# Optimization experiments

Hardware: AMD Instinct MI355X
Metric: run time of the kernel (lower is better)

## Reference

```python
import math
import jax, jax.numpy as jnp
import numpy as np


def setup_inputs() -> dict:
    key = jax.random.key(0)
    kq, kk, kv = jax.random.split(key, 3)
    bs, n_tok, n_heads, width = 2, 2048, 8, 64
    deg = 32  # neighbors per dst token -> coo_cnt_max
    q = jax.random.normal(kq, (bs, n_tok, n_heads, width), dtype=jnp.float32)
    k = jax.random.normal(kk, (bs, n_tok, n_heads, width), dtype=jnp.float32)
    v = jax.random.normal(kv, (bs, n_tok, n_heads, width), dtype=jnp.float32)
    rng = np.random.default_rng(0)
    dst = np.repeat(np.arange(n_tok), deg)            # [cl]
    src = rng.integers(0, n_tok, size=n_tok * deg)    # [cl]
    sm = np.tile(np.arange(deg), n_tok)               # [cl], unique per dst
    coo = jnp.asarray(np.stack([dst, src, sm], axis=1), dtype=jnp.int32)  # [cl,3]
    return {"q": q, "k": k, "v": v, "coo": coo, "coo_cnt_max": deg}


def reference(q, k, v, coo, coo_cnt_max):
    bs, n_tok, n_heads, width = q.shape
    dst, src, sm = coo[:, 0], coo[:, 1], coo[:, 2]
    # [b, h, t, w] layout
    qq = q.transpose(0, 2, 1, 3)
    kk = k.transpose(0, 2, 1, 3)
    vv = v.transpose(0, 2, 1, 3)
    scale = -1.0 / math.sqrt(width)
    # per-edge negative scaled L1 distance: [b, h, cl]
    ww = jnp.sum(jnp.abs(qq[:, :, dst, :] - kk[:, :, src, :]), axis=-1) * scale
    neg_big = jnp.asarray(-1e32, dtype=q.dtype)
    # scatter edge scores into dense padded attention slots: [b, h, t, cnt+1]
    attn = jnp.full((bs, n_heads, n_tok, coo_cnt_max + 1), neg_big, dtype=q.dtype)
    attn = attn.at[:, :, dst, sm].set(ww)
    attn_sm = jax.nn.softmax(attn, axis=-1)
    # scatter values into padded neighbor-value tensor: [b, h, t, cnt+1, w]
    vw = jnp.zeros((bs, n_heads, n_tok, coo_cnt_max + 1, width), dtype=q.dtype)
    vw = vw.at[:, :, dst, sm, :].set(vv[:, :, src, :])
    vo = jnp.einsum('bhds,bhdsw->bdhw', attn_sm, vw)
    # only dst tokens appearing in coo receive output; others stay zero
    vout = jnp.zeros_like(v).at[:, dst, :, :].set(vo[:, dst, :, :])
    return vout
```

## Files before the change

kernel.cpp:

```cpp
#include <hip/hip_runtime.h>

#define BS   2
#define NT   2048
#define NH   8
#define WD   64
#define DEG  32
#define HHW  (4 * WD)
#define ROWF 260

__global__ __launch_bounds__(128) void l1attn_sparse_kernel(
    const float* __restrict__ q,
    const float* __restrict__ k,
    const float* __restrict__ v,
    const int* __restrict__ coo,
    float* __restrict__ out)
{
    const int bid   = blockIdx.x;
    const int combo = bid & 3;
    const int hh    = combo & 1;
    const int b     = combo >> 1;
    const int t     = ((bid >> 3) << 1) | ((bid >> 2) & 1);
    const int tid   = threadIdx.x;
    const int hw    = tid >> 5;
    const int l     = tid & 31;

    __shared__ int   s_src[DEG];
    __shared__ float s_q[HHW];
    __shared__ float s_k[DEG * ROWF];

    if (tid < DEG) {
        s_src[tid] = coo[(t * DEG + tid) * 3 + 1];
    }
    {
        const float2* qrow = (const float2*)
            (q + ((size_t)(b * NT + t) * NH + hh * 4) * WD);
        float2 qv = qrow[tid];
        s_q[2 * tid]     = qv.x;
        s_q[2 * tid + 1] = qv.y;
    }
    __syncthreads();

    {
        const int wv = tid >> 6;
        const int ln = tid & 63;
        #pragma unroll
        for (int r = 0; r < 16; ++r) {
            const int j = wv * 16 + r;
            const int s = s_src[j];
            const float* gaddr = k + ((size_t)(b * NT + s) * NH + hh * 4) * WD
                               + ln * 4;
            float* laddr = s_k + j * ROWF;
            __builtin_amdgcn_global_load_lds(
                (const __attribute__((address_space(1))) void*)gaddr,
                (__attribute__((address_space(3))) void*)laddr,
                16, 0, 0);
        }
    }

    const int h  = hh * 4 + hw;
    const int jg = l >> 4;
    const int wq = l & 15;
    float4 vr[16];
    #pragma unroll
    for (int i = 0; i < 16; ++i) {
        const int sv = s_src[2 * i + jg];
        vr[i] = *(const float4*)(v + ((size_t)(b * NT + sv) * NH + h) * WD + 4 * wq);
    }

    __syncthreads();

    const float* qh = s_q + hw * WD;
    float acc = 0.f;
    #pragma unroll
    for (int i = 0; i < 16; ++i) {
        float4 kv = *(const float4*)(s_k + l * ROWF + hw * WD + i * 4);
        const int wb = i * 4;
        acc += fabsf(qh[wb]     - kv.x);
        acc += fabsf(qh[wb + 1] - kv.y);
        acc += fabsf(qh[wb + 2] - kv.z);
        acc += fabsf(qh[wb + 3] - kv.w);
    }
    float logit = -0.125f * acc;

    float m = logit;
    #pragma unroll
    for (int d = 16; d >= 1; d >>= 1) m = fmaxf(m, __shfl_xor(m, d));
    float e = __expf(logit - m);
    float ssum = e;
    #pragma unroll
    for (int d = 16; d >= 1; d >>= 1) ssum += __shfl_xor(ssum, d);
    const float p = e / ssum;

    float4 o4 = make_float4(0.f, 0.f, 0.f, 0.f);
    #pragma unroll
    for (int i = 0; i < 16; ++i) {
        const float pj = __shfl(p, 2 * i + jg, 32);
        o4.x += pj * vr[i].x;
        o4.y += pj * vr[i].y;
        o4.z += pj * vr[i].z;
        o4.w += pj * vr[i].w;
    }
    o4.x += __shfl_xor(o4.x, 16);
    o4.y += __shfl_xor(o4.y, 16);
    o4.z += __shfl_xor(o4.z, 16);
    o4.w += __shfl_xor(o4.w, 16);

    if (jg == 0) {
        *(float4*)(out + ((size_t)(b * NT + t) * NH + h) * WD + 4 * wq) = o4;
    }
}

extern "C" void kernel_launch(void* const* d_in, const int* in_sizes, int n_in,
                              void* d_out, int out_size, void* d_ws, size_t ws_size,
                              hipStream_t stream) {
    const float* q   = (const float*)d_in[0];
    const float* k   = (const float*)d_in[1];
    const float* v   = (const float*)d_in[2];
    const int*   coo = (const int*)d_in[3];
    float*       o   = (float*)d_out;

    dim3 grid(BS * NT * 2);
    dim3 block(128);
    hipLaunchKernelGGL(l1attn_sparse_kernel, grid, block, 0, stream, q, k, v, coo, o);
}
```

Baseline: 109.3 us.

## Use single-wave blocks over head pairs with rotated swizzled K tile in LDS

Each block now covers two heads with a single 64-thread wavefront instead of four heads with 128 threads, which doubles the grid and shrinks LDS use per block from about 33KB to about 16KB. The padded K row layout is replaced by an XOR-free rotation swizzle: each lane loads its 16-byte chunk at offset (lane+j)&31 so the direct global-to-LDS loads and later reads avoid bank conflicts without padding. The aim is more resident blocks per CU and better latency hiding. In exchange, q row and coo index loads are repeated across twice as many blocks.

```diff
diff --git a/kernel.cpp b/kernel.cpp
--- a/kernel.cpp
+++ b/kernel.cpp
@@ -5,10 +5,8 @@
 #define NH   8
 #define WD   64
 #define DEG  32
-#define HHW  (4 * WD)
-#define ROWF 260
 
-__global__ __launch_bounds__(128) void l1attn_sparse_kernel(
+__global__ __launch_bounds__(64) void l1attn_sparse_kernel(
     const float* __restrict__ q,
     const float* __restrict__ k,
     const float* __restrict__ v,
@@ -16,40 +14,40 @@
     float* __restrict__ out)
 {
     const int bid   = blockIdx.x;
-    const int combo = bid & 3;
-    const int hh    = combo & 1;
-    const int b     = combo >> 1;
-    const int t     = ((bid >> 3) << 1) | ((bid >> 2) & 1);
-    const int tid   = threadIdx.x;
-    const int hw    = tid >> 5;
-    const int l     = tid & 31;
+    const int combo = bid & 7;
+    const int hp    = combo & 3;
+    const int b     = combo >> 2;
+    const int t     = bid >> 3;
+    const int ln    = threadIdx.x;
+    const int hw    = ln >> 5;
+    const int l     = ln & 31;
 
     __shared__ int   s_src[DEG];
-    __shared__ float s_q[HHW];
-    __shared__ float s_k[DEG * ROWF];
+    __shared__ float s_q[2 * WD];
+    __shared__ float s_k[DEG * 2 * WD];
 
-    if (tid < DEG) {
-        s_src[tid] = coo[(t * DEG + tid) * 3 + 1];
+    if (ln < DEG) {
+        s_src[ln] = coo[(t * DEG + ln) * 3 + 1];
     }
     {
         const float2* qrow = (const float2*)
-            (q + ((size_t)(b * NT + t) * NH + hh * 4) * WD);
-        float2 qv = qrow[tid];
-        s_q[2 * tid]     = qv.x;
-        s_q[2 * tid + 1] = qv.y;
+            (q + ((size_t)(b * NT + t) * NH + hp * 2) * WD);
+        float2 qv = qrow[ln];
+        s_q[2 * ln]     = qv.x;
+        s_q[2 * ln + 1] = qv.y;
     }
     __syncthreads();
 
     {
-        const int wv = tid >> 6;
-        const int ln = tid & 63;
+        const int c = l;
         #pragma unroll
         for (int r = 0; r < 16; ++r) {
-            const int j = wv * 16 + r;
+            const int j = 2 * r + hw;
             const int s = s_src[j];
-            const float* gaddr = k + ((size_t)(b * NT + s) * NH + hh * 4) * WD
-                               + ln * 4;
-            float* laddr = s_k + j * ROWF;
+            const int chunk = (c + j) & 31;
+            const float* gaddr = k + ((size_t)(b * NT + s) * NH + hp * 2) * WD
+                               + chunk * 4;
+            float* laddr = s_k + 2 * r * (2 * WD);
             __builtin_amdgcn_global_load_lds(
                 (const __attribute__((address_space(1))) void*)gaddr,
                 (__attribute__((address_space(3))) void*)laddr,
@@ -57,7 +55,7 @@
         }
     }
 
-    const int h  = hh * 4 + hw;
+    const int h  = hp * 2 + hw;
     const int jg = l >> 4;
     const int wq = l & 15;
     float4 vr[16];
@@ -73,7 +71,8 @@
     float acc = 0.f;
     #pragma unroll
     for (int i = 0; i < 16; ++i) {
-        float4 kv = *(const float4*)(s_k + l * ROWF + hw * WD + i * 4);
+        const int slot = ((hw * 16 + i) - l) & 31;
+        float4 kv = *(const float4*)(s_k + l * (2 * WD) + slot * 4);
         const int wb = i * 4;
         acc += fabsf(qh[wb]     - kv.x);
         acc += fabsf(qh[wb + 1] - kv.y);
@@ -119,7 +118,7 @@
     const int*   coo = (const int*)d_in[3];
     float*       o   = (float*)d_out;
 
-    dim3 grid(BS * NT * 2);
-    dim3 block(128);
+    dim3 grid(BS * NT * 4);
+    dim3 block(64);
     hipLaunchKernelGGL(l1attn_sparse_kernel, grid, block, 0, stream, q, k, v, coo, o);
 }
```

After: 106.3 us. 2.7% less time.
